# Kernel tuning notes

Measured on AMD Instinct MI355X. Metric: run time of the kernel, lower is better.

Reference implementation:

```python
import jax, jax.numpy as jnp
import numpy as np

N_HEAD = 8
HID = 256
V_DIM = HID // N_HEAD
IN_CH = 3
OUT_CH = 1
N_BLOCKS = 4
BATCH = 4
N_FULL = 4096
N_LAT = 1024
LOCALITIES = (3.0, 5.0, 5.0, 5.0, 5.0, 3.0)


def _linear(x, w, b):
    # eqx.nn.Linear convention: w is [out, in]
    return x @ w.T + b


def _pos_att(m_dist, x, r, weight, locality):
    # m_dist: [h, Nq, Nk]; x: [b, Nk, HID]; r: [h,1,1]; weight: [h, HID, V_DIM]
    scale = jnp.tan(0.25 * jnp.pi * (1 - 1e-07) * (1 + jnp.sin(r)))  # [h,1,1]
    sd = m_dist * scale  # [h, Nq, Nk]
    if locality <= 100:
        thr = jnp.percentile(sd, locality, axis=-1, keepdims=True)
        sd = jnp.where(sd <= thr, sd, jnp.inf)
    att = jax.nn.softmax(-sd, axis=-1)  # [h, Nq, Nk]
    value = jnp.einsum('bnj,hjk->bhnk', x, weight)  # [b, h, Nk, V_DIM]
    out = jnp.einsum('hjn,bhnk->bhjk', att, value)  # [b, h, Nq, V_DIM]
    out = out.transpose(0, 2, 1, 3).reshape(out.shape[0], out.shape[2], -1)  # [b, Nq, HID]
    return jax.nn.gelu(out)


def setup_inputs():
    key = jax.random.key(0)
    ks = jax.random.split(key, 16)
    def nrm(k, shape, scale=1.0):
        return jax.random.normal(k, shape, dtype=jnp.float32) * scale
    inv = float(1.0 / np.sqrt(HID))
    return {
        'x': nrm(ks[0], (BATCH, N_FULL, IN_CH)),
        'm_dist_down': jax.random.uniform(ks[1], (N_HEAD, N_LAT, N_FULL), dtype=jnp.float32),
        'm_dist_blocks': jax.random.uniform(ks[2], (N_BLOCKS, N_HEAD, N_LAT, N_LAT), dtype=jnp.float32),
        'm_dist_up': jax.random.uniform(ks[3], (N_HEAD, N_FULL, N_LAT), dtype=jnp.float32),
        'en_w': nrm(ks[4], (HID, IN_CH), float(1.0 / np.sqrt(IN_CH))),
        'en_b': jnp.zeros((HID,), jnp.float32),
        'down_r': nrm(ks[5], (N_HEAD, 1, 1)),
        'down_w': nrm(ks[6], (N_HEAD, HID, V_DIM), inv),
        'pa_r': nrm(ks[7], (N_BLOCKS, N_HEAD, 1, 1)),
        'pa_w': nrm(ks[8], (N_BLOCKS, N_HEAD, HID, V_DIM), inv),
        'mlp1_w': nrm(ks[9], (N_BLOCKS, HID, HID), inv),
        'mlp1_b': jnp.zeros((N_BLOCKS, HID), jnp.float32),
        'mlp2_w': nrm(ks[10], (N_BLOCKS, HID, HID), inv),
        'mlp2_b': jnp.zeros((N_BLOCKS, HID), jnp.float32),
        'res_w': nrm(ks[11], (N_BLOCKS, HID, HID), inv),
        'res_b': jnp.zeros((N_BLOCKS, HID), jnp.float32),
        'up_r': nrm(ks[12], (N_HEAD, 1, 1)),
        'up_w': nrm(ks[13], (N_HEAD, HID, V_DIM), inv),
        'de1_w': nrm(ks[14], (HID, HID), inv),
        'de1_b': jnp.zeros((HID,), jnp.float32),
        'de2_w': nrm(ks[15], (OUT_CH, HID), inv),
        'de2_b': jnp.zeros((OUT_CH,), jnp.float32),
    }


def reference(x, m_dist_down, m_dist_blocks, m_dist_up, en_w, en_b, down_r, down_w,
              pa_r, pa_w, mlp1_w, mlp1_b, mlp2_w, mlp2_b, res_w, res_b,
              up_r, up_w, de1_w, de1_b, de2_w, de2_b):
    # Encoder: lift + downsampling position-attention
    h = jax.nn.gelu(_linear(x, en_w, en_b))  # [b, N_FULL, HID]
    h = _pos_att(m_dist_down, h, down_r, down_w, LOCALITIES[0])  # [b, N_LAT, HID]
    # Processor blocks: PA -> MLP, plus linear residual, gelu
    for i in range(N_BLOCKS):
        pa = _pos_att(m_dist_blocks[i], h, pa_r[i], pa_w[i], LOCALITIES[1 + i])
        mlp = _linear(jax.nn.gelu(_linear(pa, mlp1_w[i], mlp1_b[i])), mlp2_w[i], mlp2_b[i])
        h = jax.nn.gelu(mlp + _linear(h, res_w[i], res_b[i]))
    # Decoder: upsampling position-attention + projection
    h = _pos_att(m_dist_up, h, up_r, up_w, LOCALITIES[-1])  # [b, N_FULL, HID]
    h = jax.nn.gelu(_linear(h, de1_w, de1_b))
    return _linear(h, de2_w, de2_b)  # [b, N_FULL, OUT_CH]
```

## Files before the change

### kernel.cpp

```cpp
#include <hip/hip_runtime.h>
#include <math.h>


typedef short bf16x8 __attribute__((ext_vector_type(8)));
typedef float f32x4 __attribute__((ext_vector_type(4)));

__device__ __forceinline__ float gelu_f(float x) {
  float x3 = x * x * x;
  float inner = x + 0.044715f * x3;
  float t = tanhf(0.7978845608028654f * inner);
  return x * (0.5f * (1.0f + t));
}

__device__ __forceinline__ unsigned short f2bf(float x) {
  union { float f; unsigned u; } v; v.f = x;
  return (unsigned short)((v.u + 0x7fffu + ((v.u >> 16) & 1u)) >> 16);
}
__device__ __forceinline__ float bf2f(unsigned short b) {
  union { unsigned u; float f; } v; v.u = ((unsigned)b) << 16; return v.f;
}
__device__ __forceinline__ void store_bf(unsigned short* hi, unsigned short* lo,
                                         size_t i, float v) {
  unsigned short h = f2bf(v);
  hi[i] = h;
  lo[i] = f2bf(v - bf2f(h));
}

struct PrepArgs {
  const float *mlp1, *mlp2, *res, *de1, *down, *pa, *up;
  unsigned short *rm_hi, *rm_lo, *val_hi, *val_lo;
};
__global__ __launch_bounds__(256) void k_prep(PrepArgs p) {
  int i = blockIdx.x * 256 + threadIdx.x;
  if (i < 851968) {
    const float* src; int off;
    if (i < 262144)      { src = p.mlp1; off = i; }
    else if (i < 524288) { src = p.mlp2; off = i - 262144; }
    else if (i < 786432) { src = p.res;  off = i - 524288; }
    else                 { src = p.de1;  off = i - 786432; }
    float x = src[off];
    store_bf(p.rm_hi, p.rm_lo, i, x);
  } else if (i < 1245184) {
    int ii = i - 851968;
    const float* src; int off;
    if (ii < 65536)       { src = p.down; off = ii; }
    else if (ii < 327680) { src = p.pa;   off = ii - 65536; }
    else                  { src = p.up;   off = ii - 327680; }
    int m = off >> 16, rem = off & 65535;
    int o = rem >> 8, j = rem & 255;
    float x = src[(size_t)m * 65536 + (o >> 5) * 8192 + j * 32 + (o & 31)];
    store_bf(p.val_hi, p.val_lo, ii, x);
  }
}

__global__ __launch_bounds__(256) void k_lift(const float* __restrict__ x,
                                              const float* __restrict__ w,
                                              const float* __restrict__ b,
                                              unsigned short* __restrict__ ohi,
                                              unsigned short* __restrict__ olo) {
  int gid = blockIdx.x * 256 + threadIdx.x;
  int m = gid >> 8, o = gid & 255;
  float a0 = x[m * 3 + 0], a1 = x[m * 3 + 1], a2 = x[m * 3 + 2];
  float acc = a0 * w[o * 3 + 0] + a1 * w[o * 3 + 1] + a2 * w[o * 3 + 2] + b[o];
  store_bf(ohi, olo, gid, gelu_f(acc));
}

template <int ACT, int ADDRES, int OBF16>
__global__ __launch_bounds__(256) void k_gemm(
    const unsigned short* __restrict__ Ahi, const unsigned short* __restrict__ Alo,
    const unsigned short* __restrict__ Whi, const unsigned short* __restrict__ Wlo,
    const float* __restrict__ bias, const float* __restrict__ D,
    float* __restrict__ C, unsigned short* __restrict__ Chi,
    unsigned short* __restrict__ Clo) {
  int t = threadIdx.x;
  int w = t >> 6, l = t & 63;
  int m0 = blockIdx.x * 64 + (w >> 1) * 32;
  int o0 = blockIdx.y * 64 + (w & 1) * 32;
  int fr = l & 15, fq = l >> 4;
  f32x4 acc[2][2] = {};
  size_t a0 = (size_t)(m0 + fr) * 256 + fq * 8;
  size_t a1 = a0 + 16 * 256;
  size_t b0 = (size_t)(o0 + fr) * 256 + fq * 8;
  size_t b1 = b0 + 16 * 256;
  for (int ks = 0; ks < 8; ++ks) {
    int k0 = ks * 32;
    bf16x8 A0h = *(const bf16x8*)(Ahi + a0 + k0);
    bf16x8 A0l = *(const bf16x8*)(Alo + a0 + k0);
    bf16x8 A1h = *(const bf16x8*)(Ahi + a1 + k0);
    bf16x8 A1l = *(const bf16x8*)(Alo + a1 + k0);
    bf16x8 B0h = *(const bf16x8*)(Whi + b0 + k0);
    bf16x8 B0l = *(const bf16x8*)(Wlo + b0 + k0);
    bf16x8 B1h = *(const bf16x8*)(Whi + b1 + k0);
    bf16x8 B1l = *(const bf16x8*)(Wlo + b1 + k0);
#define MFMA4(ACC, AH, AL, BH, BL)                                            \
  ACC = __builtin_amdgcn_mfma_f32_16x16x32_bf16(AH, BH, ACC, 0, 0, 0);        \
  ACC = __builtin_amdgcn_mfma_f32_16x16x32_bf16(AH, BL, ACC, 0, 0, 0);        \
  ACC = __builtin_amdgcn_mfma_f32_16x16x32_bf16(AL, BH, ACC, 0, 0, 0);        \
  ACC = __builtin_amdgcn_mfma_f32_16x16x32_bf16(AL, BL, ACC, 0, 0, 0);
    MFMA4(acc[0][0], A0h, A0l, B0h, B0l)
    MFMA4(acc[0][1], A0h, A0l, B1h, B1l)
    MFMA4(acc[1][0], A1h, A1l, B0h, B0l)
    MFMA4(acc[1][1], A1h, A1l, B1h, B1l)
#undef MFMA4
  }
  float bb[2];
  bb[0] = bias ? bias[o0 + fr] : 0.0f;
  bb[1] = bias ? bias[o0 + 16 + fr] : 0.0f;
#pragma unroll
  for (int i = 0; i < 2; ++i) {
#pragma unroll
    for (int jx = 0; jx < 2; ++jx) {
      int col = o0 + jx * 16 + fr;
#pragma unroll
      for (int r = 0; r < 4; ++r) {
        int rowi = m0 + i * 16 + fq * 4 + r;
        size_t oidx = (size_t)rowi * 256 + col;
        float v = acc[i][jx][r] + bb[jx];
        if (ADDRES) v += D[oidx];
        if (ACT) v = gelu_f(v);
        if (OBF16) store_bf(Chi, Clo, oidx, v);
        else C[oidx] = v;
      }
    }
  }
}

__global__ void k_scales(const float* __restrict__ down_r,
                         const float* __restrict__ pa_r,
                         const float* __restrict__ up_r,
                         float* __restrict__ scales) {
  int t = threadIdx.x;
  if (t >= 48) return;
  float rv;
  if (t < 8) rv = down_r[t];
  else if (t < 40) rv = pa_r[t - 8];
  else rv = up_r[t - 40];
  double rd = (double)rv;
  float s1 = (float)sin(rd);
  float u = 1.0f + s1;
  float vc = (float)(0.7853981633974483 * (1.0 - 1e-7));
  float wf = vc * u;
  scales[t] = (float)tan((double)wf);
}

template <int N, int CAP>
__global__ __launch_bounds__(256) void k_wselpv(
    const float* __restrict__ mdist, const float* __restrict__ scales,
    int sc_off, int Nq, int k_lo, float hw, float lw, float frac,
    const float* __restrict__ V, int Nk,
    unsigned short* __restrict__ out_hi, unsigned short* __restrict__ out_lo) {
  constexpr int CH = N / 256;
  constexpr int SMAX = (CAP + 63) / 64;
  __shared__ float cv[4][CAP];
  __shared__ int ci[4][CAP];
  __shared__ int ccnt[4];
  __shared__ float svsel[4][2];
  __shared__ float swin[4][32];

  int tid = threadIdx.x;
  int w = tid >> 6, l = tid & 63;
  int row = blockIdx.x * 4 + w;
  int h = row / Nq, j = row - h * Nq;
  float scale = scales[sc_off + h];
  const float4* mrow4 = (const float4*)(mdist + (size_t)row * N);

  float lmin = INFINITY, lmax = -INFINITY;
#pragma unroll
  for (int e = 0; e < CH; ++e) {
    float4 v = mrow4[l + 64 * e];
    lmin = fminf(lmin, fminf(fminf(v.x, v.y), fminf(v.z, v.w)));
    lmax = fmaxf(lmax, fmaxf(fmaxf(v.x, v.y), fmaxf(v.z, v.w)));
  }
#pragma unroll
  for (int off = 32; off > 0; off >>= 1) {
    lmin = fminf(lmin, __shfl_xor(lmin, off));
    lmax = fmaxf(lmax, __shfl_xor(lmax, off));
  }
  float rmin = lmin, rmax = lmax;

  int K = 0;
  float inv_total = 1.0f;
  if (rmax > rmin) {
    float range = rmax - rmin;
    float margin = fmaxf(fabsf(rmax) * 1e-6f, 1e-30f);
    float rtop = rmax + margin;
    float wtop = rmin + range * frac;
    if (!(wtop > rmin)) wtop = rtop;
    float v_lo = rmin, v_hi = rmin;
    int count = 0;
    float xv[SMAX];
    for (int it = 0; it < 20; ++it) {
      if (l == 0) ccnt[w] = 0;
#pragma unroll
      for (int e = 0; e < CH; ++e) {
        float4 v = mrow4[l + 64 * e];
        int i0 = 4 * (l + 64 * e);
        if (v.x < wtop) { int p = atomicAdd(&ccnt[w], 1); if (p < CAP) { cv[w][p] = v.x; ci[w][p] = i0; } }
        if (v.y < wtop) { int p = atomicAdd(&ccnt[w], 1); if (p < CAP) { cv[w][p] = v.y; ci[w][p] = i0 + 1; } }
        if (v.z < wtop) { int p = atomicAdd(&ccnt[w], 1); if (p < CAP) { cv[w][p] = v.z; ci[w][p] = i0 + 2; } }
        if (v.w < wtop) { int p = atomicAdd(&ccnt[w], 1); if (p < CAP) { cv[w][p] = v.w; ci[w][p] = i0 + 3; } }
      }
      count = ccnt[w];
      if (count < k_lo + 2) { wtop = fminf(rmin + (wtop - rmin) * 3.0f, rtop); continue; }
      if (count > CAP)      { wtop = rmin + (wtop - rmin) * 0.6f; continue; }

#pragma unroll
      for (int s = 0; s < SMAX; ++s) {
        int slot = l + 64 * s;
        xv[s] = (slot < count) ? cv[w][slot] : INFINITY;
      }
      float wlo = rmin, whi = wtop;
      int rbase = 0, cntw = count;
      int found = 0, degen = 0;
      for (int bs = 0; bs < 32; ++bs) {
        if (cntw <= 24) break;
        float mid = 0.5f * (wlo + whi);
        if (!(mid > wlo && mid < whi)) { degen = 1; break; }
        int c4 = 0;
#pragma unroll
        for (int s = 0; s < SMAX; ++s) c4 += (xv[s] >= wlo && xv[s] < mid) ? 1 : 0;
#pragma unroll
        for (int off = 32; off > 0; off >>= 1) c4 += __shfl_xor(c4, off);
        int rrel = k_lo - rbase;
        if (rrel + 1 < c4) { whi = mid; cntw = c4; }
        else if (rrel >= c4) { wlo = mid; rbase += c4; cntw -= c4; }
        else {
          float mx = -INFINITY, mn = INFINITY;
#pragma unroll
          for (int s = 0; s < SMAX; ++s) {
            float v = xv[s];
            if (v >= wlo && v < mid) mx = fmaxf(mx, v);
            if (v >= mid && v < whi) mn = fminf(mn, v);
          }
#pragma unroll
          for (int off = 32; off > 0; off >>= 1) {
            mx = fmaxf(mx, __shfl_xor(mx, off));
            mn = fminf(mn, __shfl_xor(mn, off));
          }
          v_lo = mx; v_hi = mn; found = 1;
          break;
        }
      }
      if (!found) {
        if (!degen && cntw <= 32) {
          if (l == 0) ccnt[w] = 0;
#pragma unroll
          for (int s = 0; s < SMAX; ++s) {
            float v = xv[s];
            if (v >= wlo && v < whi) {
              int p = atomicAdd(&ccnt[w], 1);
              if (p < 32) swin[w][p] = v;
            }
          }
          int m = ccnt[w];
          if (m > 32) m = 32;
          float myv = (l < m) ? swin[w][l] : INFINITY;
          int clt = 0, ceq = 0;
          for (int jj = 0; jj < m; ++jj) {
            float y = swin[w][jj];
            clt += (y < myv) ? 1 : 0;
            ceq += (y == myv) ? 1 : 0;
          }
          int rr = k_lo - rbase;
          if (l < m) {
            if (clt <= rr && rr < clt + ceq) svsel[w][0] = myv;
            if (clt <= rr + 1 && rr + 1 < clt + ceq) svsel[w][1] = myv;
          }
          v_lo = svsel[w][0];
          v_hi = svsel[w][1];
        } else {
          int clt[SMAX], ceq[SMAX];
#pragma unroll
          for (int s = 0; s < SMAX; ++s) { clt[s] = 0; ceq[s] = 0; }
          for (int jj = 0; jj < count; ++jj) {
            float y = cv[w][jj];
#pragma unroll
            for (int s = 0; s < SMAX; ++s) {
              clt[s] += (y < xv[s]) ? 1 : 0;
              ceq[s] += (y == xv[s]) ? 1 : 0;
            }
          }
#pragma unroll
          for (int s = 0; s < SMAX; ++s) {
            int slot = l + 64 * s;
            if (slot < count) {
              if (clt[s] <= k_lo && k_lo < clt[s] + ceq[s]) svsel[w][0] = xv[s];
              if (clt[s] <= k_lo + 1 && k_lo + 1 < clt[s] + ceq[s]) svsel[w][1] = xv[s];
            }
          }
          v_lo = svsel[w][0];
          v_hi = svsel[w][1];
        }
      }
      float vlos0 = __fmul_rn(v_lo, scale);
      float vhis0 = __fmul_rn(v_hi, scale);
      float thr0 = __fadd_rn(__fmul_rn(vlos0, lw), __fmul_rn(vhis0, hw));
      if (__fmul_rn(wtop, scale) <= thr0) {
        wtop = fminf(rmin + (wtop - rmin) * 3.0f, rtop);
        continue;
      }
      break;
    }

    float vlos = __fmul_rn(v_lo, scale);
    float vhis = __fmul_rn(v_hi, scale);
    float thr = __fadd_rn(__fmul_rn(vlos, lw), __fmul_rn(vhis, hw));
    float rmins = __fmul_rn(rmin, scale);

    int oi[SMAX]; int kp[SMAX];
#pragma unroll
    for (int s = 0; s < SMAX; ++s) {
      int slot = l + 64 * s;
      oi[s] = 0; kp[s] = 0;
      if (slot < count) {
        oi[s] = ci[w][slot];
        kp[s] = (__fmul_rn(xv[s], scale) <= thr) ? 1 : 0;
      }
    }
    int base = 0;
    float lsum = 0.0f;
    unsigned long long mlt = (l == 0) ? 0ull : (~0ull >> (64 - l));
#pragma unroll
    for (int s = 0; s < SMAX; ++s) {
      unsigned long long bal = __ballot(kp[s] != 0);
      int pos = base + (int)__popcll(bal & mlt);
      if (kp[s]) {
        float e0 = expf(__fsub_rn(rmins, __fmul_rn(xv[s], scale)));
        cv[w][pos] = e0;
        ci[w][pos] = oi[s];
        lsum += e0;
      }
      base += (int)__popcll(bal);
    }
    K = base;
#pragma unroll
    for (int off = 32; off > 0; off >>= 1) lsum += __shfl_xor(lsum, off);
    inv_total = 1.0f / lsum;
  } else {
    K = 0;
    inv_total = 1.0f / (float)Nk;
  }

  int bh = l >> 5, c = l & 31;
  int hcol = h * 32 + c;
  const float* Vb0 = V + (size_t)bh * Nk * 256;
  const float* Vb1 = V + (size_t)(bh + 2) * Nk * 256;
  float acc0 = 0.0f, acc1 = 0.0f;
  if (K > 0) {
    for (int e = 0; e < K; ++e) {
      float we = cv[w][e];
      int n = ci[w][e];
      size_t o = (size_t)n * 256 + hcol;
      acc0 = fmaf(we, Vb0[o], acc0);
      acc1 = fmaf(we, Vb1[o], acc1);
    }
  } else {
    for (int n = 0; n < Nk; ++n) {
      size_t o = (size_t)n * 256 + hcol;
      acc0 += Vb0[o];
      acc1 += Vb1[o];
    }
  }
  size_t o0i = ((size_t)bh * Nq + j) * 256 + hcol;
  size_t o1i = ((size_t)(bh + 2) * Nq + j) * 256 + hcol;
  store_bf(out_hi, out_lo, o0i, gelu_f(acc0 * inv_total));
  store_bf(out_hi, out_lo, o1i, gelu_f(acc1 * inv_total));
}

__global__ __launch_bounds__(256) void k_de2(const float* __restrict__ A,
                                             const float* __restrict__ w,
                                             const float* __restrict__ b,
                                             float* __restrict__ out) {
  int t = threadIdx.x;
  int row = blockIdx.x * 4 + (t >> 6);
  int lane = t & 63;
  const float* ar = A + (size_t)row * 256;
  float s = 0.0f;
  for (int i = lane; i < 256; i += 64) s = fmaf(ar[i], w[i], s);
#pragma unroll
  for (int off = 32; off > 0; off >>= 1) s += __shfl_down(s, off);
  if (lane == 0) out[row] = s + b[0];
}

struct SelParams { int k_lo; float hw, lw, frac; };
static SelParams sel_params(double q, int N) {
  SelParams p;
  float idx_q = (float)(q / 100.0);
  float pos = idx_q * (float)(N - 1);
  float lo = floorf(pos);
  p.k_lo = (int)lo;
  p.hw = pos - lo;
  p.lw = 1.0f - p.hw;
  float need = (float)(p.k_lo + 2);
  p.frac = (need + 6.0f * sqrtf(need) + 8.0f) / (float)N;
  return p;
}

extern "C" void kernel_launch(void* const* d_in, const int* in_sizes, int n_in,
                              void* d_out, int out_size, void* d_ws, size_t ws_size,
                              hipStream_t stream) {
  const float* x      = (const float*)d_in[0];
  const float* mdd    = (const float*)d_in[1];
  const float* mdb    = (const float*)d_in[2];
  const float* mdu    = (const float*)d_in[3];
  const float* en_w   = (const float*)d_in[4];
  const float* en_b   = (const float*)d_in[5];
  const float* down_r = (const float*)d_in[6];
  const float* down_w = (const float*)d_in[7];
  const float* pa_r   = (const float*)d_in[8];
  const float* pa_w   = (const float*)d_in[9];
  const float* mlp1_w = (const float*)d_in[10];
  const float* mlp1_b = (const float*)d_in[11];
  const float* mlp2_w = (const float*)d_in[12];
  const float* mlp2_b = (const float*)d_in[13];
  const float* res_w  = (const float*)d_in[14];
  const float* res_b  = (const float*)d_in[15];
  const float* up_r   = (const float*)d_in[16];
  const float* up_w   = (const float*)d_in[17];
  const float* de1_w  = (const float*)d_in[18];
  const float* de1_b  = (const float*)d_in[19];
  const float* de2_w  = (const float*)d_in[20];
  const float* de2_b  = (const float*)d_in[21];
  float* out = (float*)d_out;
  char* base = (char*)d_ws;

  float* val               = (float*)base;
  float* t2                = (float*)(base + 16777216);
  unsigned short* hfull_hi = (unsigned short*)(base + 20971520);
  unsigned short* hfull_lo = (unsigned short*)(base + 29360128);
  unsigned short* paout_hi = (unsigned short*)(base + 37748736);
  unsigned short* paout_lo = (unsigned short*)(base + 46137344);
  unsigned short* hlat_hi  = (unsigned short*)(base + 54525952);
  unsigned short* hlat_lo  = (unsigned short*)(base + 56623104);
  unsigned short* t1_hi    = (unsigned short*)(base + 58720256);
  unsigned short* t1_lo    = (unsigned short*)(base + 60817408);
  unsigned short* wrm_hi   = (unsigned short*)(base + 62914560);
  unsigned short* wrm_lo   = (unsigned short*)(base + 64618496);
  unsigned short* wval_hi  = (unsigned short*)(base + 66322432);
  unsigned short* wval_lo  = (unsigned short*)(base + 67108864);
  float* scales            = (float*)(base + 67895296);

  k_scales<<<1, 64, 0, stream>>>(down_r, pa_r, up_r, scales);

  PrepArgs pa;
  pa.mlp1 = mlp1_w; pa.mlp2 = mlp2_w; pa.res = res_w; pa.de1 = de1_w;
  pa.down = down_w; pa.pa = pa_w; pa.up = up_w;
  pa.rm_hi = wrm_hi; pa.rm_lo = wrm_lo; pa.val_hi = wval_hi; pa.val_lo = wval_lo;
  k_prep<<<4864, 256, 0, stream>>>(pa);

  k_lift<<<16384, 256, 0, stream>>>(x, en_w, en_b, hfull_hi, hfull_lo);

  SelParams pd = sel_params(3.0, 4096);
  k_gemm<0, 0, 0><<<dim3(256, 4), 256, 0, stream>>>(
      hfull_hi, hfull_lo, wval_hi, wval_lo, nullptr, nullptr, val, nullptr, nullptr);
  k_wselpv<4096, 256><<<2048, 256, 0, stream>>>(
      mdd, scales, 0, 1024, pd.k_lo, pd.hw, pd.lw, pd.frac, val, 4096, hlat_hi, hlat_lo);

  SelParams pb = sel_params(5.0, 1024);
  for (int i = 0; i < 4; i++) {
    k_gemm<0, 0, 0><<<dim3(64, 4), 256, 0, stream>>>(
        hlat_hi, hlat_lo, wval_hi + 65536 + i * 65536, wval_lo + 65536 + i * 65536,
        nullptr, nullptr, val, nullptr, nullptr);
    k_wselpv<1024, 256><<<2048, 256, 0, stream>>>(
        mdb + (size_t)i * 8388608, scales, 8 + i * 8, 1024, pb.k_lo, pb.hw, pb.lw,
        pb.frac, val, 1024, paout_hi, paout_lo);
    k_gemm<1, 0, 1><<<dim3(64, 4), 256, 0, stream>>>(
        paout_hi, paout_lo, wrm_hi + i * 65536, wrm_lo + i * 65536,
        mlp1_b + i * 256, nullptr, nullptr, t1_hi, t1_lo);
    k_gemm<0, 0, 0><<<dim3(64, 4), 256, 0, stream>>>(
        hlat_hi, hlat_lo, wrm_hi + 524288 + i * 65536, wrm_lo + 524288 + i * 65536,
        res_b + i * 256, nullptr, t2, nullptr, nullptr);
    k_gemm<1, 1, 1><<<dim3(64, 4), 256, 0, stream>>>(
        t1_hi, t1_lo, wrm_hi + 262144 + i * 65536, wrm_lo + 262144 + i * 65536,
        mlp2_b + i * 256, t2, nullptr, hlat_hi, hlat_lo);
  }

  SelParams pu = sel_params(3.0, 1024);
  k_gemm<0, 0, 0><<<dim3(64, 4), 256, 0, stream>>>(
      hlat_hi, hlat_lo, wval_hi + 327680, wval_lo + 327680, nullptr, nullptr,
      val, nullptr, nullptr);
  k_wselpv<1024, 192><<<8192, 256, 0, stream>>>(
      mdu, scales, 40, 4096, pu.k_lo, pu.hw, pu.lw, pu.frac, val, 1024,
      paout_hi, paout_lo);

  k_gemm<1, 0, 0><<<dim3(256, 4), 256, 0, stream>>>(
      paout_hi, paout_lo, wrm_hi + 786432, wrm_lo + 786432, de1_b, nullptr,
      val, nullptr, nullptr);
  k_de2<<<4096, 256, 0, stream>>>(val, de2_w, de2_b, out);
}
```

Before: 548.7 us.

## Fold scales kernel into prep, vectorize PV gather, add occupancy hints

```diff
diff --git a/kernel.cpp b/kernel.cpp
--- a/kernel.cpp
+++ b/kernel.cpp
@@ -28,9 +28,26 @@
 
 struct PrepArgs {
   const float *mlp1, *mlp2, *res, *de1, *down, *pa, *up;
+  const float *down_r, *pa_r, *up_r;
   unsigned short *rm_hi, *rm_lo, *val_hi, *val_lo;
+  float* scales;
 };
 __global__ __launch_bounds__(256) void k_prep(PrepArgs p) {
+  if (blockIdx.x == 4864) {
+    int t = threadIdx.x;
+    if (t >= 48) return;
+    float rv;
+    if (t < 8) rv = p.down_r[t];
+    else if (t < 40) rv = p.pa_r[t - 8];
+    else rv = p.up_r[t - 40];
+    double rd = (double)rv;
+    float s1 = (float)sin(rd);
+    float u = 1.0f + s1;
+    float vc = (float)(0.7853981633974483 * (1.0 - 1e-7));
+    float wf = vc * u;
+    p.scales[t] = (float)tan((double)wf);
+    return;
+  }
   int i = blockIdx.x * 256 + threadIdx.x;
   if (i < 851968) {
     const float* src; int off;
@@ -125,26 +142,8 @@
   }
 }
 
-__global__ void k_scales(const float* __restrict__ down_r,
-                         const float* __restrict__ pa_r,
-                         const float* __restrict__ up_r,
-                         float* __restrict__ scales) {
-  int t = threadIdx.x;
-  if (t >= 48) return;
-  float rv;
-  if (t < 8) rv = down_r[t];
-  else if (t < 40) rv = pa_r[t - 8];
-  else rv = up_r[t - 40];
-  double rd = (double)rv;
-  float s1 = (float)sin(rd);
-  float u = 1.0f + s1;
-  float vc = (float)(0.7853981633974483 * (1.0 - 1e-7));
-  float wf = vc * u;
-  scales[t] = (float)tan((double)wf);
-}
-
-template <int N, int CAP>
-__global__ __launch_bounds__(256) void k_wselpv(
+template <int N, int CAP, int MW>
+__global__ __launch_bounds__(256, MW) void k_wselpv(
     const float* __restrict__ mdist, const float* __restrict__ scales,
     int sc_off, int Nq, int k_lo, float hw, float lw, float frac,
     const float* __restrict__ V, int Nk,
@@ -341,30 +340,28 @@
     inv_total = 1.0f / (float)Nk;
   }
 
-  int bh = l >> 5, c = l & 31;
-  int hcol = h * 32 + c;
-  const float* Vb0 = V + (size_t)bh * Nk * 256;
-  const float* Vb1 = V + (size_t)(bh + 2) * Nk * 256;
+  int b = l >> 4, c4 = (l & 15) * 2;
+  int hcol = h * 32 + c4;
+  const float* Vb = V + (size_t)b * Nk * 256;
   float acc0 = 0.0f, acc1 = 0.0f;
   if (K > 0) {
     for (int e = 0; e < K; ++e) {
       float we = cv[w][e];
       int n = ci[w][e];
-      size_t o = (size_t)n * 256 + hcol;
-      acc0 = fmaf(we, Vb0[o], acc0);
-      acc1 = fmaf(we, Vb1[o], acc1);
+      const float2 vv = *(const float2*)(Vb + (size_t)n * 256 + hcol);
+      acc0 = fmaf(we, vv.x, acc0);
+      acc1 = fmaf(we, vv.y, acc1);
     }
   } else {
     for (int n = 0; n < Nk; ++n) {
-      size_t o = (size_t)n * 256 + hcol;
-      acc0 += Vb0[o];
-      acc1 += Vb1[o];
-    }
-  }
-  size_t o0i = ((size_t)bh * Nq + j) * 256 + hcol;
-  size_t o1i = ((size_t)(bh + 2) * Nq + j) * 256 + hcol;
-  store_bf(out_hi, out_lo, o0i, gelu_f(acc0 * inv_total));
-  store_bf(out_hi, out_lo, o1i, gelu_f(acc1 * inv_total));
+      const float2 vv = *(const float2*)(Vb + (size_t)n * 256 + hcol);
+      acc0 += vv.x;
+      acc1 += vv.y;
+    }
+  }
+  size_t oidx = ((size_t)b * Nq + j) * 256 + hcol;
+  store_bf(out_hi, out_lo, oidx, gelu_f(acc0 * inv_total));
+  store_bf(out_hi, out_lo, oidx + 1, gelu_f(acc1 * inv_total));
 }
 
 __global__ __launch_bounds__(256) void k_de2(const float* __restrict__ A,
@@ -440,20 +437,20 @@
   unsigned short* wval_lo  = (unsigned short*)(base + 67108864);
   float* scales            = (float*)(base + 67895296);
 
-  k_scales<<<1, 64, 0, stream>>>(down_r, pa_r, up_r, scales);
-
   PrepArgs pa;
   pa.mlp1 = mlp1_w; pa.mlp2 = mlp2_w; pa.res = res_w; pa.de1 = de1_w;
   pa.down = down_w; pa.pa = pa_w; pa.up = up_w;
+  pa.down_r = down_r; pa.pa_r = pa_r; pa.up_r = up_r;
   pa.rm_hi = wrm_hi; pa.rm_lo = wrm_lo; pa.val_hi = wval_hi; pa.val_lo = wval_lo;
-  k_prep<<<4864, 256, 0, stream>>>(pa);
+  pa.scales = scales;
+  k_prep<<<4865, 256, 0, stream>>>(pa);
 
   k_lift<<<16384, 256, 0, stream>>>(x, en_w, en_b, hfull_hi, hfull_lo);
 
   SelParams pd = sel_params(3.0, 4096);
   k_gemm<0, 0, 0><<<dim3(256, 4), 256, 0, stream>>>(
       hfull_hi, hfull_lo, wval_hi, wval_lo, nullptr, nullptr, val, nullptr, nullptr);
-  k_wselpv<4096, 256><<<2048, 256, 0, stream>>>(
+  k_wselpv<4096, 256, 4><<<2048, 256, 0, stream>>>(
       mdd, scales, 0, 1024, pd.k_lo, pd.hw, pd.lw, pd.frac, val, 4096, hlat_hi, hlat_lo);
 
   SelParams pb = sel_params(5.0, 1024);
@@ -461,7 +458,7 @@
     k_gemm<0, 0, 0><<<dim3(64, 4), 256, 0, stream>>>(
         hlat_hi, hlat_lo, wval_hi + 65536 + i * 65536, wval_lo + 65536 + i * 65536,
         nullptr, nullptr, val, nullptr, nullptr);
-    k_wselpv<1024, 256><<<2048, 256, 0, stream>>>(
+    k_wselpv<1024, 256, 8><<<2048, 256, 0, stream>>>(
         mdb + (size_t)i * 8388608, scales, 8 + i * 8, 1024, pb.k_lo, pb.hw, pb.lw,
         pb.frac, val, 1024, paout_hi, paout_lo);
     k_gemm<1, 0, 1><<<dim3(64, 4), 256, 0, stream>>>(
@@ -479,7 +476,7 @@
   k_gemm<0, 0, 0><<<dim3(64, 4), 256, 0, stream>>>(
       hlat_hi, hlat_lo, wval_hi + 327680, wval_lo + 327680, nullptr, nullptr,
       val, nullptr, nullptr);
-  k_wselpv<1024, 192><<<8192, 256, 0, stream>>>(
+  k_wselpv<1024, 192, 8><<<8192, 256, 0, stream>>>(
       mdu, scales, 40, 4096, pu.k_lo, pu.hw, pu.lw, pu.frac, val, 1024,
       paout_hi, paout_lo);
 
```

Measured after the change: 566.7 us. 1.03x slower.
